# Performance work log

Hardware: AMD Instinct MI355X
Metric: run time of the kernel (lower is better)

## Reference

```python
import jax, jax.numpy as jnp
import numpy as np

B, S = 8, 2500
E, F = 128, 128          # embed_size, num_filter_maps
L = 8921                 # num_classes
V = 50002                # vocab_size + 2
KERNELS = (3, 5, 9)


def _conv1d_same(x, w, b):
    # x: [B, C_in, S], w: [C_out, C_in, K], b: [C_out]; 'same' padding for odd K
    k = w.shape[-1]
    pad = k // 2
    out = jax.lax.conv_general_dilated(
        x, w, window_strides=(1,), padding=[(pad, pad)],
        dimension_numbers=('NCH', 'OIH', 'NCH'))
    return out + b[None, :, None]


def setup_inputs() -> dict:
    key = jax.random.key(0)
    ks = jax.random.split(key, 12)
    inp = {
        'docs': jax.random.randint(ks[0], (B, S), 0, 50000),
        'doc_masks': jnp.ones((B, S), dtype=jnp.float32),
        'doc_lengths': jax.random.randint(ks[1], (B,), 1, S),
        'leaf_idxs': jnp.arange(L),
        'embed_w': jax.random.normal(ks[2], (V, E), dtype=jnp.float32) * 0.02,
        'word_U_w': jax.random.normal(ks[3], (L, F), dtype=jnp.float32) * 0.05,
        'final_w': jax.random.normal(ks[4], (L, F), dtype=jnp.float32) * 0.05,
        'final_b': jnp.zeros((L,), dtype=jnp.float32),
    }
    for i, k in enumerate(KERNELS):
        scale = (2.0 / (E * k)) ** 0.5
        inp[f'conv_w{k}'] = jax.random.normal(ks[5 + i], (F, E, k), dtype=jnp.float32) * scale
        inp[f'conv_b{k}'] = jnp.zeros((F,), dtype=jnp.float32)
    return inp


def reference(docs, doc_masks, doc_lengths, leaf_idxs, embed_w, word_U_w,
              final_w, final_b, conv_w3, conv_b3, conv_w5, conv_b5,
              conv_w9, conv_b9):
    # embed + transpose -> [B, E, S]  (dropout is identity at eval)
    x = embed_w[docs].transpose(0, 2, 1)
    # multi-kernel conv1d + tanh, stack, elementwise max -> [B, F, S]
    feats = jnp.stack([
        jnp.tanh(_conv1d_same(x, conv_w3, conv_b3)),
        jnp.tanh(_conv1d_same(x, conv_w5, conv_b5)),
        jnp.tanh(_conv1d_same(x, conv_w9, conv_b9)),
    ], axis=1)
    word_features = jnp.max(feats, axis=1)  # [B, F, S]
    # CAML label attention
    wu = word_U_w[leaf_idxs]                                   # [L, F]
    alpha = jax.nn.softmax(jnp.einsum('lf,bfs->bls', wu, word_features), axis=2)
    context = jnp.einsum('bls,bfs->blf', alpha, word_features)  # [B, L, F]
    y = jnp.einsum('blf,lf->bl', context, final_w) + final_b    # [B, L]
    return (y, context)
```

## Files before the change

kernel.cpp:

```cpp
#include <hip/hip_runtime.h>
#include <hip/hip_bf16.h>

#define BB 8
#define SS 2500
#define EE 128
#define FF 128
#define LL 8921

using bf8 = __attribute__((ext_vector_type(8))) short;
using bf4 = __attribute__((ext_vector_type(4))) short;
using f4  = __attribute__((ext_vector_type(4))) float;

__device__ __forceinline__ short f2bf(float f) {
  unsigned u = __builtin_bit_cast(unsigned, f);
  u += 0x7fffu + ((u >> 16) & 1u);
  return (short)(u >> 16);
}

__device__ __forceinline__ void gll16(const void* g, void* l) {
  __builtin_amdgcn_global_load_lds(
      (const __attribute__((address_space(1))) unsigned int*)g,
      (__attribute__((address_space(3))) unsigned int*)l, 16, 0, 0);
}

template <int CTRL>
__device__ __forceinline__ float dppmv(float x) {
  int r = __builtin_amdgcn_update_dpp(0, __builtin_bit_cast(int, x), CTRL, 0xF, 0xF, false);
  return __builtin_bit_cast(float, r);
}
__device__ __forceinline__ float rowsum16(float x) {
  x += dppmv<0xB1>(x);
  x += dppmv<0x4E>(x);
  x += dppmv<0x124>(x);
  x += dppmv<0x128>(x);
  return x;
}

__global__ void prep_kernel(const int* __restrict__ docs, const int* __restrict__ leaf,
                            const float* __restrict__ embed, const float* __restrict__ wu,
                            const float* __restrict__ w3, const float* __restrict__ w5,
                            const float* __restrict__ w9,
                            short* __restrict__ x_bf, short* __restrict__ wu_bf,
                            short* __restrict__ wpack) {
  const int NX = BB * SS * EE / 8;
  const int NU = LL * FF / 8;
  const int NW = 17 * FF * EE;
  int tid = blockIdx.x * 256 + threadIdx.x;
  if (tid < NX) {
    int base = tid * 8;
    int bs = base >> 7, e0 = base & 127;
    int row = docs[bs];
    const float* p = embed + (row << 7) + e0;
    bf8 o;
#pragma unroll
    for (int i = 0; i < 8; ++i) o[i] = f2bf(p[i]);
    *(bf8*)(x_bf + base) = o;
  } else if (tid < NX + NU) {
    int base = (tid - NX) * 8;
    int l = base >> 7, f0 = base & 127;
    int row = leaf[l];
    const float* p = wu + (row << 7) + f0;
    bf8 o;
#pragma unroll
    for (int i = 0; i < 8; ++i) o[i] = f2bf(p[i]);
    *(bf8*)(wu_bf + base) = o;
  } else if (tid < NX + NU + NW) {
    int i = tid - NX - NU;
    int t = i >> 14, fe = i & 16383;
    const float* w; int K, dk;
    if (t < 3)      { w = w3; K = 3; dk = t; }
    else if (t < 8) { w = w5; K = 5; dk = t - 3; }
    else            { w = w9; K = 9; dk = t - 8; }
    wpack[i] = f2bf(w[fe * K + dk]);
  }
}

__global__ __launch_bounds__(256, 2) void conv_kernel(
    const short* __restrict__ x_bf, const short* __restrict__ wpack,
    const float* __restrict__ cb3, const float* __restrict__ cb5, const float* __restrict__ cb9,
    short* __restrict__ wf, short* __restrict__ wfT) {
  __shared__ short xt[72][136];
  __shared__ short wt[128][136];
  int b = blockIdx.x;
  int s0 = blockIdx.y * 64;
  int tid = threadIdx.x, wid = tid >> 6, lane = tid & 63, g = lane >> 4, c = lane & 15;

  for (int i = tid; i < 72 * 16; i += 256) {
    int r = i >> 4, c8 = (i & 15) << 3, s = s0 + r - 4;
    bf8 v = {0, 0, 0, 0, 0, 0, 0, 0};
    if (s >= 0 && s < SS) v = *(const bf8*)(x_bf + ((b * SS + s) << 7) + c8);
    *(bf8*)&xt[r][c8] = v;
  }

  bf8 wpre[8];
#pragma unroll
  for (int k = 0; k < 8; ++k) {
    int i = tid + (k << 8); int r = i >> 4, c8 = (i & 15) << 3;
    wpre[k] = *(const bf8*)(wpack + (r << 7) + c8);
  }

  float wfm[8][4];
#pragma unroll
  for (int j = 0; j < 8; ++j)
#pragma unroll
    for (int i = 0; i < 4; ++i) wfm[j][i] = -1e30f;

  int tap = 0;
  for (int kid = 0; kid < 3; ++kid) {
    const float* cb = (kid == 0) ? cb3 : (kid == 1) ? cb5 : cb9;
    const int K = (kid == 0) ? 3 : (kid == 1) ? 5 : 9;
    const int pad = K >> 1;
    f4 acc[8];
#pragma unroll
    for (int j = 0; j < 8; ++j) {
      float bvj = cb[j * 16 + c];
      acc[j] = (f4){bvj, bvj, bvj, bvj};
    }
    for (int dk = 0; dk < K; ++dk, ++tap) {
      __syncthreads();
#pragma unroll
      for (int k = 0; k < 8; ++k) {
        int i = tid + (k << 8); int r = i >> 4, c8 = (i & 15) << 3;
        *(bf8*)&wt[r][c8] = wpre[k];
      }
      if (tap < 16) {
#pragma unroll
        for (int k = 0; k < 8; ++k) {
          int i = tid + (k << 8); int r = i >> 4, c8 = (i & 15) << 3;
          wpre[k] = *(const bf8*)(wpack + (tap + 1) * 16384 + (r << 7) + c8);
        }
      }
      __syncthreads();
      int xr = wid * 16 + c + dk - pad + 4;
      __builtin_amdgcn_s_setprio(1);
#pragma unroll
      for (int ks = 0; ks < 4; ++ks) {
        bf8 a = *(const bf8*)&xt[xr][ks * 32 + g * 8];
#pragma unroll
        for (int j = 0; j < 8; ++j) {
          bf8 bb = *(const bf8*)&wt[j * 16 + c][ks * 32 + g * 8];
          acc[j] = __builtin_amdgcn_mfma_f32_16x16x32_bf16(a, bb, acc[j], 0, 0, 0);
        }
      }
      __builtin_amdgcn_s_setprio(0);
    }
#pragma unroll
    for (int j = 0; j < 8; ++j)
#pragma unroll
      for (int i = 0; i < 4; ++i) wfm[j][i] = fmaxf(wfm[j][i], tanhf(acc[j][i]));
  }

  int sb = s0 + wid * 16 + g * 4;
#pragma unroll
  for (int j = 0; j < 8; ++j) {
    int f = j * 16 + c;
#pragma unroll
    for (int i = 0; i < 4; ++i) {
      int s = sb + i;
      if (s < SS) wf[((b * SS + s) << 7) + f] = f2bf(wfm[j][i]);
    }
    int tbase = (b * 128 + f) * SS + sb;
    if (sb + 3 < SS) {
      bf4 pk;
#pragma unroll
      for (int i = 0; i < 4; ++i) pk[i] = f2bf(wfm[j][i]);
      *(bf4*)(wfT + tbase) = pk;
    } else {
#pragma unroll
      for (int i = 0; i < 4; ++i)
        if (sb + i < SS) wfT[tbase + i] = f2bf(wfm[j][i]);
    }
  }
}

__global__ __launch_bounds__(256, 3) void attn_kernel(
    const short* __restrict__ wu_bf, const short* __restrict__ wf, const short* __restrict__ wfT,
    const float* __restrict__ fw, const float* __restrict__ fb,
    float* __restrict__ y, float* __restrict__ ctx) {
  __shared__ short kt[64 * 128];
  __shared__ short vt[128 * 64];
  __shared__ short pt[128][68];
  int b = blockIdx.x;
  int l0 = blockIdx.y * 128;
  int tid = threadIdx.x, wid = tid >> 6, lane = tid & 63, g = lane >> 4, c = lane & 15;

  int k_row[4], k_off[4], v_off[4];
#pragma unroll
  for (int k = 0; k < 4; ++k) {
    int idx = (k * 4 + wid) * 64 + lane;
    int r = idx >> 4, ck = idx & 15;
    k_row[k] = r;
    k_off[k] = (ck ^ (r & 15)) << 3;
    int rv = idx >> 3, cv = idx & 7;
    v_off[k] = (b * 128 + rv) * SS + ((cv ^ (rv & 7)) << 3);
  }
  const short* wfb = wf + b * SS * 128;

  bf8 q[2][4];
#pragma unroll
  for (int ms = 0; ms < 2; ++ms) {
    int l = l0 + wid * 32 + ms * 16 + c;
    if (l >= LL) l = LL - 1;
#pragma unroll
    for (int ks = 0; ks < 4; ++ks)
      q[ms][ks] = *(const bf8*)(wu_bf + (l << 7) + ks * 32 + g * 8);
  }

  float lst[2][4];
  f4 o[2][8];
#pragma unroll
  for (int ms = 0; ms < 2; ++ms) {
#pragma unroll
    for (int i = 0; i < 4; ++i) lst[ms][i] = 0.0f;
#pragma unroll
    for (int n = 0; n < 8; ++n) o[ms][n] = (f4){0.f, 0.f, 0.f, 0.f};
  }

  for (int t = 0; t < 40; ++t) {
    int s0 = t * 64;
    bool full = (s0 + 64 <= SS);
    __syncthreads();
#pragma unroll
    for (int k = 0; k < 4; ++k) {
      int s = s0 + k_row[k];
      if (s > SS - 1) s = SS - 1;
      gll16(wfb + s * 128 + k_off[k], (char*)kt + (k * 4 + wid) * 1024);
    }
    if (full) {
#pragma unroll
      for (int k = 0; k < 4; ++k)
        gll16(wfT + v_off[k] + s0, (char*)vt + (k * 4 + wid) * 1024);
    } else {
      for (int idx = tid; idx < 128 * 64; idx += 256) {
        int r = idx >> 6, sl = idx & 63, so = s0 + sl;
        short v = (so < SS) ? wfT[(b * 128 + r) * SS + so] : (short)0;
        vt[(r << 6) + (((sl >> 3) ^ (r & 7)) << 3) + (sl & 7)] = v;
      }
    }
    __syncthreads();

    float rs[2][4] = {{0.f, 0.f, 0.f, 0.f}, {0.f, 0.f, 0.f, 0.f}};
#pragma unroll
    for (int jh = 0; jh < 2; ++jh) {
      f4 sc[2][2];
#pragma unroll
      for (int ms = 0; ms < 2; ++ms)
#pragma unroll
        for (int jj = 0; jj < 2; ++jj) sc[ms][jj] = (f4){0.f, 0.f, 0.f, 0.f};
      __builtin_amdgcn_s_setprio(1);
#pragma unroll
      for (int ks = 0; ks < 4; ++ks) {
        int xk = (((ks << 2) | g) ^ c) << 3;
        bf8 kb[2];
#pragma unroll
        for (int jj = 0; jj < 2; ++jj)
          kb[jj] = *(const bf8*)&kt[((jh * 2 + jj) * 16 + c) * 128 + xk];
#pragma unroll
        for (int ms = 0; ms < 2; ++ms)
#pragma unroll
          for (int jj = 0; jj < 2; ++jj)
            sc[ms][jj] = __builtin_amdgcn_mfma_f32_16x16x32_bf16(q[ms][ks], kb[jj], sc[ms][jj], 0, 0, 0);
      }
      __builtin_amdgcn_s_setprio(0);
#pragma unroll
      for (int jj = 0; jj < 2; ++jj) {
        int j = jh * 2 + jj;
        int col = j * 16 + c;
        bool masked = (!full) && (s0 + col >= SS);
#pragma unroll
        for (int ms = 0; ms < 2; ++ms) {
          int rbase = wid * 32 + ms * 16 + g * 4;
#pragma unroll
          for (int i = 0; i < 4; ++i) {
            float p = masked ? 0.0f : __expf(sc[ms][jj][i]);
            pt[rbase + i][col] = f2bf(p);
            rs[ms][i] += p;
          }
        }
      }
    }
#pragma unroll
    for (int ms = 0; ms < 2; ++ms)
#pragma unroll
      for (int i = 0; i < 4; ++i) lst[ms][i] += rowsum16(rs[ms][i]);
    asm volatile("s_waitcnt lgkmcnt(0)" ::: "memory");
    __builtin_amdgcn_sched_barrier(0);

    __builtin_amdgcn_s_setprio(1);
#pragma unroll
    for (int ks = 0; ks < 2; ++ks) {
      bf8 pa[2];
#pragma unroll
      for (int ms = 0; ms < 2; ++ms) {
        const short* pp = &pt[wid * 32 + ms * 16 + c][ks * 32 + g * 8];
        bf4 lo = *(const bf4*)pp; bf4 hi = *(const bf4*)(pp + 4);
        pa[ms] = __builtin_shufflevector(lo, hi, 0, 1, 2, 3, 4, 5, 6, 7);
      }
      int xv = (((ks << 2) | g) ^ (c & 7)) << 3;
#pragma unroll
      for (int n = 0; n < 8; ++n) {
        bf8 vb = *(const bf8*)&vt[(n * 16 + c) * 64 + xv];
#pragma unroll
        for (int ms = 0; ms < 2; ++ms)
          o[ms][n] = __builtin_amdgcn_mfma_f32_16x16x32_bf16(pa[ms], vb, o[ms][n], 0, 0, 0);
      }
    }
    __builtin_amdgcn_s_setprio(0);
  }

#pragma unroll
  for (int ms = 0; ms < 2; ++ms)
#pragma unroll
    for (int i = 0; i < 4; ++i) {
      int l = l0 + wid * 32 + ms * 16 + g * 4 + i;
      if (l < LL) {
        float inv = 1.0f / lst[ms][i];
        int rb = (b * LL + l) << 7;
        float acc = 0.0f;
#pragma unroll
        for (int n = 0; n < 8; ++n) {
          float cv = o[ms][n][i] * inv;
          ctx[rb + n * 16 + c] = cv;
          acc += cv * fw[(l << 7) + n * 16 + c];
        }
        acc = rowsum16(acc);
        if (c == 0) y[b * LL + l] = acc + fb[l];
      }
    }
}

extern "C" void kernel_launch(void* const* d_in, const int* in_sizes, int n_in,
                              void* d_out, int out_size, void* d_ws, size_t ws_size,
                              hipStream_t stream) {
  const int* docs = (const int*)d_in[0];
  const int* leaf = (const int*)d_in[3];
  const float* embed = (const float*)d_in[4];
  const float* wu = (const float*)d_in[5];
  const float* fw = (const float*)d_in[6];
  const float* fb = (const float*)d_in[7];
  const float* w3 = (const float*)d_in[8];
  const float* b3 = (const float*)d_in[9];
  const float* w5 = (const float*)d_in[10];
  const float* b5 = (const float*)d_in[11];
  const float* w9 = (const float*)d_in[12];
  const float* b9 = (const float*)d_in[13];

  char* ws = (char*)d_ws;
  short* x_bf  = (short*)(ws);
  short* wu_bf = (short*)(ws + 5120000);
  short* wpack = (short*)(ws + 7403776);
  short* wfp   = (short*)(ws + 7960832);
  short* wfT   = (short*)(ws + 13080832);

  float* y = (float*)d_out;
  float* ctx = (float*)d_out + BB * LL;

  prep_kernel<<<2896, 256, 0, stream>>>(docs, leaf, embed, wu, w3, w5, w9, x_bf, wu_bf, wpack);
  conv_kernel<<<dim3(8, 40), 256, 0, stream>>>(x_bf, wpack, b3, b5, b9, wfp, wfT);
  attn_kernel<<<dim3(8, 70), 256, 0, stream>>>(wu_bf, wfp, wfT, fw, fb, y, ctx);
}
```

Measured before the change: 208.4 us.

## Keep softmax probabilities in registers by transposing score MFMA layout

The score MFMA now computes S^T (keys as A operand, queries as B), so each lane's exp'd probabilities already match the B-operand layout of a 16x16x16 bf16 MFMA for the PV product. This removes the shared-memory round trip for P, the pt array, and the lgkmcnt wait before PV. Row sums become per-lane partials reduced once at the end with shuffles, and the epilogue writes context as float4 vectors. The cost is twice as many smaller (16x16x16) MFMAs for PV and narrower bf4 loads of V.

Result: slower. 254.8 us (+22.3%).

```diff
diff --git a/kernel.cpp b/kernel.cpp
--- a/kernel.cpp
+++ b/kernel.cpp
@@ -21,19 +21,6 @@
   __builtin_amdgcn_global_load_lds(
       (const __attribute__((address_space(1))) unsigned int*)g,
       (__attribute__((address_space(3))) unsigned int*)l, 16, 0, 0);
-}
-
-template <int CTRL>
-__device__ __forceinline__ float dppmv(float x) {
-  int r = __builtin_amdgcn_update_dpp(0, __builtin_bit_cast(int, x), CTRL, 0xF, 0xF, false);
-  return __builtin_bit_cast(float, r);
-}
-__device__ __forceinline__ float rowsum16(float x) {
-  x += dppmv<0xB1>(x);
-  x += dppmv<0x4E>(x);
-  x += dppmv<0x124>(x);
-  x += dppmv<0x128>(x);
-  return x;
 }
 
 __global__ void prep_kernel(const int* __restrict__ docs, const int* __restrict__ leaf,
@@ -179,7 +166,6 @@
     float* __restrict__ y, float* __restrict__ ctx) {
   __shared__ short kt[64 * 128];
   __shared__ short vt[128 * 64];
-  __shared__ short pt[128][68];
   int b = blockIdx.x;
   int l0 = blockIdx.y * 128;
   int tid = threadIdx.x, wid = tid >> 6, lane = tid & 63, g = lane >> 4, c = lane & 15;
@@ -206,15 +192,12 @@
       q[ms][ks] = *(const bf8*)(wu_bf + (l << 7) + ks * 32 + g * 8);
   }
 
-  float lst[2][4];
+  float lst[2] = {0.f, 0.f};
   f4 o[2][8];
 #pragma unroll
-  for (int ms = 0; ms < 2; ++ms) {
-#pragma unroll
-    for (int i = 0; i < 4; ++i) lst[ms][i] = 0.0f;
+  for (int ms = 0; ms < 2; ++ms)
 #pragma unroll
     for (int n = 0; n < 8; ++n) o[ms][n] = (f4){0.f, 0.f, 0.f, 0.f};
-  }
 
   for (int t = 0; t < 40; ++t) {
     int s0 = t * 64;
@@ -239,94 +222,90 @@
     }
     __syncthreads();
 
-    float rs[2][4] = {{0.f, 0.f, 0.f, 0.f}, {0.f, 0.f, 0.f, 0.f}};
-#pragma unroll
-    for (int jh = 0; jh < 2; ++jh) {
+#pragma unroll
+    for (int sh = 0; sh < 2; ++sh) {
       f4 sc[2][2];
 #pragma unroll
-      for (int ms = 0; ms < 2; ++ms)
-#pragma unroll
-        for (int jj = 0; jj < 2; ++jj) sc[ms][jj] = (f4){0.f, 0.f, 0.f, 0.f};
+      for (int st2 = 0; st2 < 2; ++st2)
+#pragma unroll
+        for (int ms = 0; ms < 2; ++ms) sc[st2][ms] = (f4){0.f, 0.f, 0.f, 0.f};
       __builtin_amdgcn_s_setprio(1);
 #pragma unroll
       for (int ks = 0; ks < 4; ++ks) {
         int xk = (((ks << 2) | g) ^ c) << 3;
-        bf8 kb[2];
-#pragma unroll
-        for (int jj = 0; jj < 2; ++jj)
-          kb[jj] = *(const bf8*)&kt[((jh * 2 + jj) * 16 + c) * 128 + xk];
-#pragma unroll
-        for (int ms = 0; ms < 2; ++ms)
-#pragma unroll
-          for (int jj = 0; jj < 2; ++jj)
-            sc[ms][jj] = __builtin_amdgcn_mfma_f32_16x16x32_bf16(q[ms][ks], kb[jj], sc[ms][jj], 0, 0, 0);
+        bf8 ka[2];
+#pragma unroll
+        for (int st2 = 0; st2 < 2; ++st2)
+          ka[st2] = *(const bf8*)&kt[(((sh * 2 + st2) * 16) + c) * 128 + xk];
+#pragma unroll
+        for (int st2 = 0; st2 < 2; ++st2)
+#pragma unroll
+          for (int ms = 0; ms < 2; ++ms)
+            sc[st2][ms] = __builtin_amdgcn_mfma_f32_16x16x32_bf16(ka[st2], q[ms][ks], sc[st2][ms], 0, 0, 0);
       }
       __builtin_amdgcn_s_setprio(0);
-#pragma unroll
-      for (int jj = 0; jj < 2; ++jj) {
-        int j = jh * 2 + jj;
-        int col = j * 16 + c;
-        bool masked = (!full) && (s0 + col >= SS);
+
+#pragma unroll
+      for (int st2 = 0; st2 < 2; ++st2) {
+        int st = sh * 2 + st2;
+        bf4 pb[2];
 #pragma unroll
         for (int ms = 0; ms < 2; ++ms) {
-          int rbase = wid * 32 + ms * 16 + g * 4;
-#pragma unroll
-          for (int i = 0; i < 4; ++i) {
-            float p = masked ? 0.0f : __expf(sc[ms][jj][i]);
-            pt[rbase + i][col] = f2bf(p);
-            rs[ms][i] += p;
+          f4 p;
+          if (full) {
+#pragma unroll
+            for (int i = 0; i < 4; ++i) p[i] = __expf(sc[st2][ms][i]);
+          } else {
+#pragma unroll
+            for (int i = 0; i < 4; ++i) {
+              int s = s0 + st * 16 + (g << 2) + i;
+              p[i] = (s < SS) ? __expf(sc[st2][ms][i]) : 0.0f;
+            }
           }
+          lst[ms] += p[0] + p[1] + p[2] + p[3];
+#pragma unroll
+          for (int i = 0; i < 4; ++i) pb[ms][i] = f2bf(p[i]);
         }
-      }
-    }
-#pragma unroll
-    for (int ms = 0; ms < 2; ++ms)
-#pragma unroll
-      for (int i = 0; i < 4; ++i) lst[ms][i] += rowsum16(rs[ms][i]);
-    asm volatile("s_waitcnt lgkmcnt(0)" ::: "memory");
-    __builtin_amdgcn_sched_barrier(0);
-
-    __builtin_amdgcn_s_setprio(1);
-#pragma unroll
-    for (int ks = 0; ks < 2; ++ks) {
-      bf8 pa[2];
-#pragma unroll
-      for (int ms = 0; ms < 2; ++ms) {
-        const short* pp = &pt[wid * 32 + ms * 16 + c][ks * 32 + g * 8];
-        bf4 lo = *(const bf4*)pp; bf4 hi = *(const bf4*)(pp + 4);
-        pa[ms] = __builtin_shufflevector(lo, hi, 0, 1, 2, 3, 4, 5, 6, 7);
-      }
-      int xv = (((ks << 2) | g) ^ (c & 7)) << 3;
+        __builtin_amdgcn_s_setprio(1);
+#pragma unroll
+        for (int n = 0; n < 8; ++n) {
+          int col = st * 16 + (g << 2);
+          int off = (((col >> 3) ^ (c & 7)) << 3) + (col & 7);
+          bf4 vb = *(const bf4*)&vt[(n * 16 + c) * 64 + off];
+#pragma unroll
+          for (int ms = 0; ms < 2; ++ms)
+            o[ms][n] = __builtin_amdgcn_mfma_f32_16x16x16bf16_1k(vb, pb[ms], o[ms][n], 0, 0, 0);
+        }
+        __builtin_amdgcn_s_setprio(0);
+      }
+    }
+  }
+
+#pragma unroll
+  for (int ms = 0; ms < 2; ++ms) {
+    float lt = lst[ms];
+    lt += __shfl_xor(lt, 16);
+    lt += __shfl_xor(lt, 32);
+    int l = l0 + wid * 32 + ms * 16 + c;
+    if (l < LL) {
+      float inv = 1.0f / lt;
+      int rb = (b * LL + l) << 7;
+      float acc = 0.0f;
 #pragma unroll
       for (int n = 0; n < 8; ++n) {
-        bf8 vb = *(const bf8*)&vt[(n * 16 + c) * 64 + xv];
-#pragma unroll
-        for (int ms = 0; ms < 2; ++ms)
-          o[ms][n] = __builtin_amdgcn_mfma_f32_16x16x32_bf16(pa[ms], vb, o[ms][n], 0, 0, 0);
-      }
-    }
-    __builtin_amdgcn_s_setprio(0);
-  }
-
-#pragma unroll
-  for (int ms = 0; ms < 2; ++ms)
-#pragma unroll
-    for (int i = 0; i < 4; ++i) {
-      int l = l0 + wid * 32 + ms * 16 + g * 4 + i;
-      if (l < LL) {
-        float inv = 1.0f / lst[ms][i];
-        int rb = (b * LL + l) << 7;
-        float acc = 0.0f;
-#pragma unroll
-        for (int n = 0; n < 8; ++n) {
-          float cv = o[ms][n][i] * inv;
-          ctx[rb + n * 16 + c] = cv;
-          acc += cv * fw[(l << 7) + n * 16 + c];
-        }
-        acc = rowsum16(acc);
-        if (c == 0) y[b * LL + l] = acc + fb[l];
-      }
-    }
+        f4 cv;
+#pragma unroll
+        for (int i = 0; i < 4; ++i) cv[i] = o[ms][n][i] * inv;
+        int fo = n * 16 + (g << 2);
+        *(f4*)&ctx[rb + fo] = cv;
+        const f4 fwv = *(const f4*)&fw[(l << 7) + fo];
+        acc += cv[0] * fwv[0] + cv[1] * fwv[1] + cv[2] * fwv[2] + cv[3] * fwv[3];
+      }
+      acc += __shfl_xor(acc, 16);
+      acc += __shfl_xor(acc, 32);
+      if (g == 0) y[b * LL + l] = acc + fb[l];
+    }
+  }
 }
 
 extern "C" void kernel_launch(void* const* d_in, const int* in_sizes, int n_in,
```
